# Kernel tuning notes

Hardware: AMD Instinct MI355X
Metric: run time of the kernel (lower is better)

## Reference

```python
import jax, jax.numpy as jnp
import numpy as np

TEMPERATURE = 1.0
EPS = 1e-8
B, D, N, K = 2048, 32, 8192, 30


def setup_inputs() -> dict:
    key = jax.random.key(0)
    k1, k2, k3 = jax.random.split(key, 3)
    z_current = jax.random.normal(k1, (B, D), dtype=jnp.float32)
    pre_knn_indices = jax.random.randint(k2, (N, K), 0, N, dtype=jnp.int64 if jax.config.jax_enable_x64 else jnp.int32)
    sample_indices = jax.random.randint(k3, (B,), 0, N, dtype=jnp.int64 if jax.config.jax_enable_x64 else jnp.int32)
    return {"z_current": z_current, "pre_knn_indices": pre_knn_indices, "sample_indices": sample_indices}


def reference(z_current, pre_knn_indices, sample_indices):
    b = z_current.shape[0]
    eye = jnp.eye(b, dtype=bool)
    # pairwise Euclidean distance via gram trick: (B,B), avoids (B,B,D) intermediate
    sq = jnp.sum(z_current * z_current, axis=-1)
    d2 = jnp.maximum(sq[:, None] + sq[None, :] - 2.0 * (z_current @ z_current.T), 0.0)
    d2_safe = jnp.where(eye, 1.0, d2)  # avoid sqrt(0) on diagonal (masked below anyway)
    dist = jnp.sqrt(d2_safe)
    sim = jnp.where(eye, -jnp.inf, -dist / TEMPERATURE)
    soft_neighbors = jax.nn.softmax(sim, axis=1)  # (B,B)
    # neighbor mask: j is kept iff global id of j is in pre-kNN set of i, and j != i
    knn = pre_knn_indices[sample_indices]  # (B,K) global ids of i's pre-neighbors
    in_set = (knn[:, :, None] == sample_indices[None, None, :]).any(axis=1)  # (B,B)
    mask = in_set & ~eye
    s = jnp.sum(soft_neighbors * mask, axis=1)  # (B,)
    valid = mask.any(axis=1)
    count = valid.sum()
    loss_i = -jnp.log(s + EPS)
    total = jnp.sum(jnp.where(valid, loss_i, 0.0))
    return jnp.where(count > 0, total / count, jnp.float32(0.0))
```

## Files before the change

### kernel.cpp

```cpp
#include <hip/hip_runtime.h>
#include <math.h>

#define Bsz 2048
#define Ddim 32
#define Nsz 8192
#define Kk 30
#define TPB 256
#define ROWS 4
#define JSL 2
#define JTILE (Bsz / JSL)
#define JCH (JTILE / TPB)
#define NBLK ((Bsz / ROWS) * JSL)
#define NW (Nsz / 32)

__global__ __launch_bounds__(TPB, 2) void softnp_main(
    const float* __restrict__ z,
    const int*   __restrict__ pre_knn,
    const int*   __restrict__ samp,
    float*       __restrict__ wsden,
    float*       __restrict__ wsnum)
{
    __shared__ unsigned bits4[NW][ROWS];
    __shared__ int      sampsh[JTILE];
    __shared__ float    zish[ROWS * Ddim];
    __shared__ int      rowsi[ROWS];
    __shared__ float    rden[4][ROWS], rnum[4][ROWS];

    const int t  = threadIdx.x;
    const int rg = blockIdx.x >> 1;
    const int sl = blockIdx.x & 1;
    const int i0 = rg * ROWS;
    const int jb = sl * JTILE;

    #pragma unroll
    for (int c = 0; c < (NW * ROWS) / TPB; ++c)
        ((unsigned*)bits4)[t + c * TPB] = 0u;
    #pragma unroll
    for (int c = 0; c < JCH; ++c)
        sampsh[t + c * TPB] = samp[jb + t + c * TPB];
    if (t < ROWS * Ddim) zish[t] = z[(size_t)i0 * Ddim + t];
    if (t < ROWS) rowsi[t] = samp[i0 + t];
    __syncthreads();

    if (t < ROWS * 32) {
        const int r = t >> 5, k = t & 31;
        if (k < Kk) {
            const int id = pre_knn[(size_t)rowsi[r] * Kk + k];
            atomicOr(&bits4[id >> 5][r], 1u << (id & 31));
        }
    }

    float4 zi[ROWS][Ddim / 4];
    const float4* z4 = (const float4*)zish;
    #pragma unroll
    for (int r = 0; r < ROWS; ++r)
        #pragma unroll
        for (int d = 0; d < Ddim / 4; ++d)
            zi[r][d] = z4[r * (Ddim / 4) + d];

    float si2[ROWS];
    #pragma unroll
    for (int r = 0; r < ROWS; ++r) {
        float s = 0.f;
        #pragma unroll
        for (int d = 0; d < Ddim / 4; ++d)
            s += zi[r][d].x * zi[r][d].x + zi[r][d].y * zi[r][d].y
               + zi[r][d].z * zi[r][d].z + zi[r][d].w * zi[r][d].w;
        si2[r] = s;
    }
    __syncthreads();

    float den[ROWS] = {0.f, 0.f, 0.f, 0.f};
    float num[ROWS] = {0.f, 0.f, 0.f, 0.f};

    const float4* zg = (const float4*)z;
    int j = jb + t;
    float4 cur[8];
    #pragma unroll
    for (int d = 0; d < 8; ++d) cur[d] = zg[(size_t)j * 8 + d];

    #pragma unroll
    for (int c = 0; c < JCH; ++c) {
        float4 nxt[8];
        if (c + 1 < JCH) {
            #pragma unroll
            for (int d = 0; d < 8; ++d) nxt[d] = zg[(size_t)(j + TPB) * 8 + d];
        }

        float dot[ROWS] = {0.f, 0.f, 0.f, 0.f};
        float sj2 = 0.f;
        #pragma unroll
        for (int d = 0; d < 8; ++d) {
            const float4 v = cur[d];
            sj2 += v.x * v.x + v.y * v.y + v.z * v.z + v.w * v.w;
            #pragma unroll
            for (int r = 0; r < ROWS; ++r)
                dot[r] += zi[r][d].x * v.x + zi[r][d].y * v.y
                        + zi[r][d].z * v.z + zi[r][d].w * v.w;
        }

        const int   sj = sampsh[t + c * TPB];
        const uint4 bw = ((const uint4*)bits4)[sj >> 5];
        const unsigned bsel[4] = {bw.x, bw.y, bw.z, bw.w};
        #pragma unroll
        for (int r = 0; r < ROWS; ++r) {
            const float d2 = fmaxf(si2[r] + sj2 - 2.f * dot[r], 0.f);
            const bool diag = (j == i0 + r);
            const float e = diag ? 0.f : __expf(-sqrtf(d2));
            den[r] += e;
            if (!diag && ((bsel[r] >> (sj & 31)) & 1u)) num[r] += e;
        }

        if (c + 1 < JCH) {
            #pragma unroll
            for (int d = 0; d < 8; ++d) cur[d] = nxt[d];
        }
        j += TPB;
    }

    const int lane = t & 63, wv = t >> 6;
    #pragma unroll
    for (int r = 0; r < ROWS; ++r) {
        #pragma unroll
        for (int off = 32; off > 0; off >>= 1) {
            den[r] += __shfl_xor(den[r], off, 64);
            num[r] += __shfl_xor(num[r], off, 64);
        }
    }
    if (lane == 0) {
        #pragma unroll
        for (int r = 0; r < ROWS; ++r) { rden[wv][r] = den[r]; rnum[wv][r] = num[r]; }
    }
    __syncthreads();

    if (t < ROWS) {
        float D = 0.f, Nm = 0.f;
        #pragma unroll
        for (int w = 0; w < 4; ++w) { D += rden[w][t]; Nm += rnum[w][t]; }
        wsden[sl * Bsz + i0 + t] = D;
        wsnum[sl * Bsz + i0 + t] = Nm;
    }
}

__global__ __launch_bounds__(TPB) void softnp_final(
    const float* __restrict__ wsden,
    const float* __restrict__ wsnum,
    float*       __restrict__ out)
{
    __shared__ float rl[4], rc[4];
    const int t = threadIdx.x;
    float loss = 0.f, vcnt = 0.f;
    #pragma unroll
    for (int c = 0; c < Bsz / TPB; ++c) {
        const int r = t + c * TPB;
        const float D  = wsden[r] + wsden[Bsz + r];
        const float Nm = wsnum[r] + wsnum[Bsz + r];
        if (Nm > 0.f) {
            loss -= __logf(Nm / D + 1e-8f);
            vcnt += 1.f;
        }
    }
    #pragma unroll
    for (int off = 32; off > 0; off >>= 1) {
        loss += __shfl_xor(loss, off, 64);
        vcnt += __shfl_xor(vcnt, off, 64);
    }
    const int lane = t & 63, wv = t >> 6;
    if (lane == 0) { rl[wv] = loss; rc[wv] = vcnt; }
    __syncthreads();
    if (t == 0) {
        const float L = rl[0] + rl[1] + rl[2] + rl[3];
        const float C = rc[0] + rc[1] + rc[2] + rc[3];
        out[0] = (C > 0.f) ? L / C : 0.f;
    }
}

extern "C" void kernel_launch(void* const* d_in, const int* in_sizes, int n_in,
                              void* d_out, int out_size, void* d_ws, size_t ws_size,
                              hipStream_t stream)
{
    const float* z       = (const float*)d_in[0];
    const int*   pre_knn = (const int*)d_in[1];
    const int*   samp    = (const int*)d_in[2];
    float*       out     = (float*)d_out;
    float*       wsden   = (float*)d_ws;
    float*       wsnum   = wsden + JSL * Bsz;

    softnp_main<<<dim3(NBLK), dim3(TPB), 0, stream>>>(z, pre_knn, samp, wsden, wsnum);
    softnp_final<<<dim3(1), dim3(TPB), 0, stream>>>(wsden, wsnum, out);
}
```

Measured before the change: 84.52 us.

## Use 2 rows per block over full j range with scalarized row vectors

Each block now handles 2 query rows over all 2048 columns instead of 4 rows over half the columns, which removes the column split and the two-part reduction in the final kernel. The row vectors and their squared norms are made wave-uniform with readfirstlane so they can sit in scalar registers, cutting vector register pressure, and launch bounds now ask for 3 blocks per SM. The trade-off is that every column vector of z is read from global memory twice as often across blocks, and the row-side math does less reuse per column load.

```diff
diff --git a/kernel.cpp b/kernel.cpp
--- a/kernel.cpp
+++ b/kernel.cpp
@@ -6,38 +6,37 @@
 #define Nsz 8192
 #define Kk 30
 #define TPB 256
-#define ROWS 4
-#define JSL 2
-#define JTILE (Bsz / JSL)
-#define JCH (JTILE / TPB)
-#define NBLK ((Bsz / ROWS) * JSL)
+#define ROWS 2
+#define NBLK (Bsz / ROWS)
+#define JCH (Bsz / TPB)
 #define NW (Nsz / 32)
 
-__global__ __launch_bounds__(TPB, 2) void softnp_main(
+__device__ __forceinline__ float rfl(float x) {
+    return __uint_as_float(__builtin_amdgcn_readfirstlane(__float_as_uint(x)));
+}
+
+__global__ __launch_bounds__(TPB, 3) void softnp_main(
     const float* __restrict__ z,
     const int*   __restrict__ pre_knn,
     const int*   __restrict__ samp,
     float*       __restrict__ wsden,
     float*       __restrict__ wsnum)
 {
-    __shared__ unsigned bits4[NW][ROWS];
-    __shared__ int      sampsh[JTILE];
+    __shared__ unsigned bits2[NW][ROWS];
+    __shared__ int      sampsh[Bsz];
     __shared__ float    zish[ROWS * Ddim];
     __shared__ int      rowsi[ROWS];
     __shared__ float    rden[4][ROWS], rnum[4][ROWS];
 
     const int t  = threadIdx.x;
-    const int rg = blockIdx.x >> 1;
-    const int sl = blockIdx.x & 1;
-    const int i0 = rg * ROWS;
-    const int jb = sl * JTILE;
+    const int i0 = blockIdx.x * ROWS;
 
     #pragma unroll
     for (int c = 0; c < (NW * ROWS) / TPB; ++c)
-        ((unsigned*)bits4)[t + c * TPB] = 0u;
+        ((unsigned*)bits2)[t + c * TPB] = 0u;
     #pragma unroll
     for (int c = 0; c < JCH; ++c)
-        sampsh[t + c * TPB] = samp[jb + t + c * TPB];
+        sampsh[t + c * TPB] = samp[t + c * TPB];
     if (t < ROWS * Ddim) zish[t] = z[(size_t)i0 * Ddim + t];
     if (t < ROWS) rowsi[t] = samp[i0 + t];
     __syncthreads();
@@ -46,35 +45,32 @@
         const int r = t >> 5, k = t & 31;
         if (k < Kk) {
             const int id = pre_knn[(size_t)rowsi[r] * Kk + k];
-            atomicOr(&bits4[id >> 5][r], 1u << (id & 31));
+            atomicOr(&bits2[id >> 5][r], 1u << (id & 31));
         }
     }
+    __syncthreads();
 
-    float4 zi[ROWS][Ddim / 4];
-    const float4* z4 = (const float4*)zish;
+    float zis[ROWS][Ddim];
     #pragma unroll
     for (int r = 0; r < ROWS; ++r)
         #pragma unroll
-        for (int d = 0; d < Ddim / 4; ++d)
-            zi[r][d] = z4[r * (Ddim / 4) + d];
+        for (int d = 0; d < Ddim; ++d)
+            zis[r][d] = rfl(zish[r * Ddim + d]);
 
     float si2[ROWS];
     #pragma unroll
     for (int r = 0; r < ROWS; ++r) {
         float s = 0.f;
         #pragma unroll
-        for (int d = 0; d < Ddim / 4; ++d)
-            s += zi[r][d].x * zi[r][d].x + zi[r][d].y * zi[r][d].y
-               + zi[r][d].z * zi[r][d].z + zi[r][d].w * zi[r][d].w;
-        si2[r] = s;
+        for (int d = 0; d < Ddim; ++d) s += zis[r][d] * zis[r][d];
+        si2[r] = rfl(s);
     }
-    __syncthreads();
 
-    float den[ROWS] = {0.f, 0.f, 0.f, 0.f};
-    float num[ROWS] = {0.f, 0.f, 0.f, 0.f};
+    float den[ROWS] = {0.f, 0.f};
+    float num[ROWS] = {0.f, 0.f};
 
     const float4* zg = (const float4*)z;
-    int j = jb + t;
+    int j = t;
     float4 cur[8];
     #pragma unroll
     for (int d = 0; d < 8; ++d) cur[d] = zg[(size_t)j * 8 + d];
@@ -87,7 +83,7 @@
             for (int d = 0; d < 8; ++d) nxt[d] = zg[(size_t)(j + TPB) * 8 + d];
         }
 
-        float dot[ROWS] = {0.f, 0.f, 0.f, 0.f};
+        float dot[ROWS] = {0.f, 0.f};
         float sj2 = 0.f;
         #pragma unroll
         for (int d = 0; d < 8; ++d) {
@@ -95,13 +91,13 @@
             sj2 += v.x * v.x + v.y * v.y + v.z * v.z + v.w * v.w;
             #pragma unroll
             for (int r = 0; r < ROWS; ++r)
-                dot[r] += zi[r][d].x * v.x + zi[r][d].y * v.y
-                        + zi[r][d].z * v.z + zi[r][d].w * v.w;
+                dot[r] += zis[r][4 * d + 0] * v.x + zis[r][4 * d + 1] * v.y
+                        + zis[r][4 * d + 2] * v.z + zis[r][4 * d + 3] * v.w;
         }
 
-        const int   sj = sampsh[t + c * TPB];
-        const uint4 bw = ((const uint4*)bits4)[sj >> 5];
-        const unsigned bsel[4] = {bw.x, bw.y, bw.z, bw.w};
+        const int   sj = sampsh[j];
+        const uint2 bw = ((const uint2*)bits2)[sj >> 5];
+        const unsigned bsel[2] = {bw.x, bw.y};
         #pragma unroll
         for (int r = 0; r < ROWS; ++r) {
             const float d2 = fmaxf(si2[r] + sj2 - 2.f * dot[r], 0.f);
@@ -137,8 +133,8 @@
         float D = 0.f, Nm = 0.f;
         #pragma unroll
         for (int w = 0; w < 4; ++w) { D += rden[w][t]; Nm += rnum[w][t]; }
-        wsden[sl * Bsz + i0 + t] = D;
-        wsnum[sl * Bsz + i0 + t] = Nm;
+        wsden[i0 + t] = D;
+        wsnum[i0 + t] = Nm;
     }
 }
 
@@ -153,8 +149,8 @@
     #pragma unroll
     for (int c = 0; c < Bsz / TPB; ++c) {
         const int r = t + c * TPB;
-        const float D  = wsden[r] + wsden[Bsz + r];
-        const float Nm = wsnum[r] + wsnum[Bsz + r];
+        const float D  = wsden[r];
+        const float Nm = wsnum[r];
         if (Nm > 0.f) {
             loss -= __logf(Nm / D + 1e-8f);
             vcnt += 1.f;
@@ -184,7 +180,7 @@
     const int*   samp    = (const int*)d_in[2];
     float*       out     = (float*)d_out;
     float*       wsden   = (float*)d_ws;
-    float*       wsnum   = wsden + JSL * Bsz;
+    float*       wsnum   = wsden + Bsz;
 
     softnp_main<<<dim3(NBLK), dim3(TPB), 0, stream>>>(z, pre_knn, samp, wsden, wsnum);
     softnp_final<<<dim3(1), dim3(TPB), 0, stream>>>(wsden, wsnum, out);
```

Result: slower. 93.88 us (+11.1%).
